# Kernel optimization log

Hardware: AMD Instinct MI355X
Metric: run time of the kernel (lower is better)

## Reference

```python
import jax, jax.numpy as jnp
import numpy as np
from math import factorial

NODES = 40000      # number of nodes
EDGES = 640000     # number of edges (avg degree 16)
MUL = 8            # multiplicity of each irrep in hidden (8x0e+8x1e+8x2e)
NB = 16            # radial basis size (radial_neurons[0])
MAXR = 3.0         # max_radius
NSPECIES = 8
DEG = 16.0         # num_neighbors normalization
R8 = 1.0 / np.sqrt(8.0)

# ---------- real Clebsch-Gordan coefficients (precomputed with numpy) ----------
def _clebsch(j1, m1, j2, m2, j3, m3):
    f = factorial
    if m1 + m2 != m3:
        return 0.0
    pref = ((2*j3+1) * f(j3+j1-j2) * f(j3-j1+j2) * f(j1+j2-j3) / f(j1+j2+j3+1)) ** 0.5
    pref *= (f(j3+m3)*f(j3-m3)*f(j1-m1)*f(j1+m1)*f(j2-m2)*f(j2+m2)) ** 0.5
    lo = max(0, j2-j3-m1, j1-j3+m2)
    hi = min(j1+j2-j3, j1-m1, j2+m2)
    s = 0.0
    for k in range(lo, hi+1):
        s += (-1)**k / (f(k)*f(j1+j2-j3-k)*f(j1-m1-k)*f(j2+m2-k)*f(j3-j2+m1+k)*f(j3-j1-m2+k))
    return pref * s

def _U(l):
    # complex -> real spherical-harmonic change of basis (rows: real m, cols: complex m)
    U = np.zeros((2*l+1, 2*l+1), dtype=complex)
    s2 = 2 ** -0.5
    for m in range(-l, l+1):
        if m > 0:
            U[m+l, m+l] = (-1)**m * s2; U[m+l, -m+l] = s2
        elif m == 0:
            U[l, l] = 1.0
        else:
            U[m+l, m+l] = 1j*s2; U[m+l, -m+l] = -1j*((-1)**m)*s2
    return U

def _real_cg(l1, l2, l3):
    C = np.zeros((2*l1+1, 2*l2+1, 2*l3+1))
    for m1 in range(-l1, l1+1):
        for m2 in range(-l2, l2+1):
            m3 = m1 + m2
            if abs(m3) <= l3:
                C[m1+l1, m2+l2, m3+l3] = _clebsch(l1, m1, l2, m2, l3, m3)
    T = np.einsum('am,bn,co,mno->abc', _U(l1).conj(), _U(l2).conj(), _U(l3), C)
    R = T.imag if np.abs(T.imag).max() > np.abs(T.real).max() else T.real
    return jnp.asarray(R.astype(np.float32))

PATHS = [(0,0,0),(0,1,1),(0,2,2),(1,0,1),(1,1,0),(1,1,1),(1,1,2),
         (1,2,1),(1,2,2),(2,0,2),(2,1,1),(2,1,2),(2,2,0),(2,2,1),(2,2,2)]
CG = {p: _real_cg(*p) for p in PATHS}
NIN = {0: 3.0, 1: 6.0, 2: 6.0}  # fan-in path counts per output l in hidden convs

# ---------- irrep feature layout: [.., 72] = 8x0e | 8x1e | 8x2e ----------
def _split(h):
    lead = h.shape[:-1]
    return (h[..., :MUL],
            h[..., MUL:4*MUL].reshape(lead + (MUL, 3)),
            h[..., 4*MUL:].reshape(lead + (MUL, 5)))

def _merge(s, v, t):
    lead = s.shape[:-1]
    return jnp.concatenate([s, v.reshape(lead + (3*MUL,)), t.reshape(lead + (5*MUL,))], -1)

def _act(h):
    # e3nn Activation: silu on 0e scalars, identity on l>0
    s, v, t = _split(h)
    return _merge(jax.nn.silu(s), v, t)

def _radial(emb, w1, b1, w2, b2):
    return jax.nn.silu(emb @ w1 + b1) @ w2 + b2

def _sh(u):
    # component-normalized real spherical harmonics l=0,1,2 of unit vectors u [E,3]
    x, y, z = u[:, 0], u[:, 1], u[:, 2]
    c15 = np.sqrt(15.0); c5 = np.sqrt(5.0); c3 = np.sqrt(3.0)
    y1 = jnp.stack([y, z, x], -1) * c3
    y2 = jnp.stack([c15*x*y, c15*y*z, 0.5*c5*(3*z*z - 1.0), c15*x*z, 0.5*c15*(x*x - y*y)], -1)
    return jnp.concatenate([jnp.ones_like(x)[:, None], y1, y2], -1)

def _soft_onehot(r):
    # e3nn soft_one_hot_linspace, basis='smooth_finite', cutoff=True
    values = jnp.linspace(0.0, MAXR, NB + 2)[1:-1]
    step = MAXR / (NB + 1)
    d = (r[:, None] - values) / step
    inside = jnp.abs(d) < 1.0
    dd = jnp.where(inside, d, 0.0)
    f = jnp.exp(-1.0 / (1.0 + dd)) * jnp.exp(-1.0 / (1.0 - dd))
    return 1.14136 * np.exp(2.0) * jnp.where(inside, f, 0.0)

def _tp_first(hs, sh, w):
    # uvu TP: 8x0e (x) SH(1x0e+1x1e+1x2e) -> hidden; hs [E,8], sh [E,9], w [E,3,8]
    m_s = w[:, 0] * hs * sh[:, :1]
    m_v = w[:, 1][..., None] * hs[..., None] * sh[:, None, 1:4]
    m_t = w[:, 2][..., None] * hs[..., None] * sh[:, None, 4:9]
    return _merge(m_s, m_v, m_t)

def _tp_uuu(h1, h2, w):
    # depthwise (uuu) CG tensor product hidden (x) hidden -> hidden; w [E,15,8]
    s1, v1, t1 = _split(h1); s2, v2, t2 = _split(h2)
    a = {0: s1[..., None], 1: v1, 2: t1}
    b = {0: s2[..., None], 1: v2, 2: t2}
    out = {0: 0.0, 1: 0.0, 2: 0.0}
    for p, (l1, l2, l3) in enumerate(PATHS):
        out[l3] = out[l3] + w[:, p, :, None] * jnp.einsum('eci,ecj,ijk->eck', a[l1], b[l2], CG[(l1, l2, l3)])
    return _merge(out[0][..., 0] / np.sqrt(NIN[0]), out[1] / np.sqrt(NIN[1]), out[2] / np.sqrt(NIN[2]))

def _lin_hidden(h, lin):
    # irrep-wise linear self-connection, lin [3,8,8]
    s, v, t = _split(h)
    return _merge(s @ lin[0] * R8,
                  jnp.einsum('ncm,cd->ndm', v, lin[1]) * R8,
                  jnp.einsum('ncm,cd->ndm', t, lin[2]) * R8)

def _model(x, edge_index, edge_vec, embed_w, lin0, lin1, lin2, out_w,
           r0_w1, r0_b1, r0_w2, r0_b2, r1_w1, r1_b1, r1_w2, r1_b2,
           r2_w1, r2_b1, r2_w2, r2_b2):
    src, dst = edge_index[0], edge_index[1]
    h = embed_w[x]                                   # [N, 8] scalar node feats
    r = jnp.sqrt(jnp.sum(edge_vec**2, -1) + 1e-12)
    emb = _soft_onehot(r)                            # [E, 16]
    hb_sh = _sh(edge_vec / r[:, None])               # [E, 9]
    rdeg = 1.0 / np.sqrt(DEG)
    # conv 0 + activation
    w = _radial(emb, r0_w1, r0_b1, r0_w2, r0_b2).reshape(-1, 3, MUL)
    m = _tp_first(h[src], hb_sh, w)                  # [E, 72]
    agg = jax.ops.segment_sum(m, dst, num_segments=NODES) * rdeg
    h = _act(agg.at[:, :MUL].add((h @ lin0) * R8))
    hb = _act(m)
    # convs 1..2 + activation
    for (w1, b1, w2, b2, lin) in ((r1_w1, r1_b1, r1_w2, r1_b2, lin1),
                                  (r2_w1, r2_b1, r2_w2, r2_b2, lin2)):
        w = _radial(emb, w1, b1, w2, b2).reshape(-1, 15, MUL)
        m = _tp_uuu(h[src], hb, w)
        agg = jax.ops.segment_sum(m, dst, num_segments=NODES) * rdeg
        h = _act(_lin_hidden(h, lin) + agg)
        hb = _act(m)
    # output FullyConnectedTensorProduct(h, h) -> 8x0e (paths l(x)l->0)
    s, v, t = _split(h)
    i0 = s[:, :, None] * s[:, None, :]
    i1 = jnp.einsum('nim,njm->nij', v, v) / np.sqrt(3.0)
    i2 = jnp.einsum('nim,njm->nij', t, t) / np.sqrt(5.0)
    out = (jnp.einsum('nij,ijk->nk', i0, out_w[0])
           + jnp.einsum('nij,ijk->nk', i1, out_w[1])
           + jnp.einsum('nij,ijk->nk', i2, out_w[2])) / np.sqrt(3.0 * MUL * MUL)
    return out

def setup_inputs() -> dict:
    key = jax.random.key(0)
    ks = jax.random.split(key, 16)
    inp = {}
    inp['x'] = jax.random.randint(ks[0], (NODES,), 0, NSPECIES)
    inp['edge_index'] = jax.random.randint(ks[1], (2, EDGES), 0, NODES)
    inp['edge_vec'] = jax.random.normal(ks[2], (EDGES, 3), dtype=jnp.float32)
    inp['embed_w'] = jax.random.normal(ks[3], (NSPECIES, MUL), dtype=jnp.float32)
    inp['lin0'] = jax.random.normal(ks[4], (MUL, MUL), dtype=jnp.float32)
    inp['lin1'] = jax.random.normal(ks[5], (3, MUL, MUL), dtype=jnp.float32)
    inp['lin2'] = jax.random.normal(ks[6], (3, MUL, MUL), dtype=jnp.float32)
    inp['out_w'] = jax.random.normal(ks[7], (3, MUL, MUL, MUL), dtype=jnp.float32)
    for i, (name, od) in enumerate((('r0', 3*MUL), ('r1', 15*MUL), ('r2', 15*MUL))):
        k1, k2 = jax.random.split(ks[8+i])
        inp[name+'_w1'] = jax.random.normal(k1, (NB, 64), dtype=jnp.float32) / np.sqrt(NB)
        inp[name+'_b1'] = jnp.zeros((64,), dtype=jnp.float32)
        inp[name+'_w2'] = jax.random.normal(k2, (64, od), dtype=jnp.float32) / 8.0
        inp[name+'_b2'] = jnp.zeros((od,), dtype=jnp.float32)
    return inp

def reference(x, edge_index, edge_vec, embed_w, lin0, lin1, lin2, out_w,
              r0_w1, r0_b1, r0_w2, r0_b2, r1_w1, r1_b1, r1_w2, r1_b2,
              r2_w1, r2_b1, r2_w2, r2_b2):
    return _model(x, edge_index, edge_vec, embed_w, lin0, lin1, lin2, out_w,
                  r0_w1, r0_b1, r0_w2, r0_b2, r1_w1, r1_b1, r1_w2, r1_b2,
                  r2_w1, r2_b1, r2_w2, r2_b2)
```

## Files before the change

### kernel.cpp

```cpp
#include <hip/hip_runtime.h>

#define NODES 40000
#define EDGES 640000

typedef float f32x2v __attribute__((ext_vector_type(2)));
typedef float f32x4v __attribute__((ext_vector_type(4)));
typedef short short8v __attribute__((ext_vector_type(8)));

__device__ __forceinline__ float silu_f(float x) { return x / (1.0f + __expf(-x)); }
__device__ __forceinline__ f32x2v mk2(float a, float b) { f32x2v r; r[0] = a; r[1] = b; return r; }

__device__ __forceinline__ void tp_uuu2(const f32x2v* wv,
                                        f32x2v as, const f32x2v* av, const f32x2v* at,
                                        f32x2v bs, const f32x2v* bv, const f32x2v* bt,
                                        f32x2v& ms, f32x2v* mv, f32x2v* mt)
{
    const float CR = 0.70710678f;
    const float K1 = 0.31622777f;
    const float K3 = 0.54772256f;
    const float KA = 0.40824829f;
    const float KB = 0.70710678f;
    const float KC = 0.81649658f;
    const float L4 = 0.63245553f;
    const float G2 = 0.53452248f;
    const float G1 = 0.26726124f;
    const float HH = 0.46291005f;

    f32x2v os = {0.f, 0.f};
    f32x2v ov0 = {0.f, 0.f}, ov1 = {0.f, 0.f}, ov2 = {0.f, 0.f};
    f32x2v ot0 = {0.f, 0.f}, ot1 = {0.f, 0.f}, ot2 = {0.f, 0.f};
    f32x2v ot3 = {0.f, 0.f}, ot4 = {0.f, 0.f};

    os += wv[0] * as * bs;
    ov0 += wv[1] * as * bv[0]; ov1 += wv[1] * as * bv[1]; ov2 += wv[1] * as * bv[2];
    ot0 += wv[2] * as * bt[0]; ot1 += wv[2] * as * bt[1]; ot2 += wv[2] * as * bt[2];
    ot3 += wv[2] * as * bt[3]; ot4 += wv[2] * as * bt[4];
    ov0 += wv[3] * av[0] * bs; ov1 += wv[3] * av[1] * bs; ov2 += wv[3] * av[2] * bs;
    os += wv[4] * (-0.57735027f) * (av[0]*bv[0] + av[1]*bv[1] + av[2]*bv[2]);
    ov0 += wv[5] * CR * (av[1]*bv[2] - av[2]*bv[1]);
    ov1 += wv[5] * CR * (av[2]*bv[0] - av[0]*bv[2]);
    ov2 += wv[5] * CR * (av[0]*bv[1] - av[1]*bv[0]);
    ot0 += wv[6] * CR * (av[2]*bv[0] + av[0]*bv[2]);
    ot1 += wv[6] * CR * (av[0]*bv[1] + av[1]*bv[0]);
    ot2 += wv[6] * 0.40824829f * (2.f*av[1]*bv[1] - av[2]*bv[2] - av[0]*bv[0]);
    ot3 += wv[6] * CR * (av[2]*bv[1] + av[1]*bv[2]);
    ot4 += wv[6] * CR * (av[2]*bv[2] - av[0]*bv[0]);
    ov0 += wv[7] * (-K3*av[1]*bt[1] + K1*av[0]*bt[2] - K3*av[2]*bt[0] + K3*av[0]*bt[4]);
    ov1 += wv[7] * (-2.f*K1*av[1]*bt[2] - K3*av[2]*bt[3] - K3*av[0]*bt[1]);
    ov2 += wv[7] * (-K3*av[1]*bt[3] + K1*av[2]*bt[2] - K3*av[0]*bt[0] - K3*av[2]*bt[4]);
    ot0 += wv[8] * ( KC*av[1]*bt[4] - KA*av[2]*bt[3] + KA*av[0]*bt[1]);
    ot1 += wv[8] * ( KA*av[1]*bt[3] - KB*av[2]*bt[2] - KA*av[0]*bt[0] - KA*av[2]*bt[4]);
    ot2 += wv[8] * ( KB*av[2]*bt[1] - KB*av[0]*bt[3]);
    ot3 += wv[8] * (-KA*av[1]*bt[1] + KB*av[0]*bt[2] + KA*av[2]*bt[0] - KA*av[0]*bt[4]);
    ot4 += wv[8] * (-KC*av[1]*bt[0] + KA*av[2]*bt[1] + KA*av[0]*bt[3]);
    ot0 += wv[9] * at[0] * bs; ot1 += wv[9] * at[1] * bs; ot2 += wv[9] * at[2] * bs;
    ot3 += wv[9] * at[3] * bs; ot4 += wv[9] * at[4] * bs;
    ov0 += wv[10] * (-K3*bv[1]*at[1] + K1*bv[0]*at[2] - K3*bv[2]*at[0] + K3*bv[0]*at[4]);
    ov1 += wv[10] * (-2.f*K1*bv[1]*at[2] - K3*bv[2]*at[3] - K3*bv[0]*at[1]);
    ov2 += wv[10] * (-K3*bv[1]*at[3] + K1*bv[2]*at[2] - K3*bv[0]*at[0] - K3*bv[2]*at[4]);
    ot0 -= wv[11] * ( KC*bv[1]*at[4] - KA*bv[2]*at[3] + KA*bv[0]*at[1]);
    ot1 -= wv[11] * ( KA*bv[1]*at[3] - KB*bv[2]*at[2] - KA*bv[0]*at[0] - KA*bv[2]*at[4]);
    ot2 -= wv[11] * ( KB*bv[2]*at[1] - KB*bv[0]*at[3]);
    ot3 -= wv[11] * (-KA*bv[1]*at[1] + KB*bv[0]*at[2] + KA*bv[2]*at[0] - KA*bv[0]*at[4]);
    ot4 -= wv[11] * (-KC*bv[1]*at[0] + KA*bv[2]*at[1] + KA*bv[0]*at[3]);
    os += wv[12] * 0.44721360f * (at[0]*bt[0] + at[1]*bt[1] + at[2]*bt[2] + at[3]*bt[3] + at[4]*bt[4]);
    ov0 += wv[13] * ( K1*(at[0]*bt[1] - at[1]*bt[0]) + K3*(at[3]*bt[2] - at[2]*bt[3]) + K1*(at[4]*bt[3] - at[3]*bt[4]) );
    ov1 += wv[13] * ( L4*(at[0]*bt[4] - at[4]*bt[0]) + K1*(at[1]*bt[3] - at[3]*bt[1]) );
    ov2 += wv[13] * ( K1*(at[3]*bt[0] - at[0]*bt[3]) + K3*(at[2]*bt[1] - at[1]*bt[2]) + K1*(at[4]*bt[1] - at[1]*bt[4]) );
    ot0 += wv[14] * ( G2*(at[2]*bt[0] + at[0]*bt[2]) - HH*(at[1]*bt[3] + at[3]*bt[1]) );
    ot1 += wv[14] * (-HH*(at[3]*bt[0] + at[0]*bt[3]) + HH*(at[1]*bt[4] + at[4]*bt[1]) - G1*(at[2]*bt[1] + at[1]*bt[2]) );
    ot2 += wv[14] * ( G2*(at[0]*bt[0] + at[4]*bt[4] - at[2]*bt[2]) - G1*(at[1]*bt[1] + at[3]*bt[3]) );
    ot3 += wv[14] * (-HH*(at[1]*bt[0] + at[0]*bt[1]) - HH*(at[3]*bt[4] + at[4]*bt[3]) - G1*(at[2]*bt[3] + at[3]*bt[2]) );
    ot4 += wv[14] * ( G2*(at[2]*bt[4] + at[4]*bt[2]) + HH*(at[1]*bt[1] - at[3]*bt[3]) );

    ms = os * 0.57735027f;
    mv[0] = ov0 * 0.40824829f; mv[1] = ov1 * 0.40824829f; mv[2] = ov2 * 0.40824829f;
    mt[0] = ot0 * 0.40824829f; mt[1] = ot1 * 0.40824829f; mt[2] = ot2 * 0.40824829f;
    mt[3] = ot3 * 0.40824829f; mt[4] = ot4 * 0.40824829f;
}

__global__ void deg_kernel(const int* __restrict__ eidx, int* __restrict__ deg)
{
    int e = blockIdx.x * 256 + threadIdx.x;
    if (e < EDGES) atomicAdd(&deg[eidx[EDGES + e]], 1);
}

__launch_bounds__(1024)
__global__ void scan_kernel(const int* __restrict__ deg, int* __restrict__ off,
                            int* __restrict__ cursor)
{
    __shared__ int part[1024];
    const int t = threadIdx.x;
    const int base = t * 40;
    int v[40];
    if (t < 1000) {
        const int4* p4 = (const int4*)(deg + base);
        #pragma unroll
        for (int i = 0; i < 10; ++i) {
            int4 q = p4[i];
            v[4 * i + 0] = q.x; v[4 * i + 1] = q.y;
            v[4 * i + 2] = q.z; v[4 * i + 3] = q.w;
        }
    } else {
        #pragma unroll
        for (int i = 0; i < 40; ++i) v[i] = 0;
    }
    int loc[40];
    int s = 0;
    #pragma unroll
    for (int i = 0; i < 40; ++i) { loc[i] = s; s += v[i]; }
    part[t] = s;
    __syncthreads();
    for (int d = 1; d < 1024; d <<= 1) {
        int vv = (t >= d) ? part[t - d] : 0;
        __syncthreads();
        part[t] += vv;
        __syncthreads();
    }
    int tb = (t == 0) ? 0 : part[t - 1];
    if (t < 1000) {
        #pragma unroll
        for (int i = 0; i < 40; ++i) {
            off[base + i] = tb + loc[i];
            cursor[base + i] = tb + loc[i];
        }
    }
    if (t == 1023) off[NODES] = part[1023];
}

__global__ void build_kernel(const int* __restrict__ eidx, const float* __restrict__ ev,
                             int* __restrict__ cursor,
                             float* __restrict__ evp, int* __restrict__ srcs)
{
    int e = blockIdx.x * 256 + threadIdx.x;
    if (e < EDGES) {
        int dst = eidx[EDGES + e];
        int p = atomicAdd(&cursor[dst], 1);
        srcs[p] = (int)(((unsigned)eidx[e]) | ((unsigned)dst << 16));
        evp[p * 3 + 0] = ev[e * 3 + 0];
        evp[p * 3 + 1] = ev[e * 3 + 1];
        evp[p * 3 + 2] = ev[e * 3 + 2];
    }
}

__launch_bounds__(256, 3)
__global__ void layer0_edge(const float* __restrict__ evp, const int* __restrict__ srcs,
                            const int* __restrict__ xs, const float* __restrict__ embw,
                            const float* __restrict__ w1, const float* __restrict__ b1,
                            const float* __restrict__ w2, const float* __restrict__ b2,
                            float* __restrict__ mbuf)
{
    __shared__ float emb_s[128 * 17];
    __shared__ float hid_s[128 * 68];
    __shared__ float w2t[24 * 68];
    const int tid = threadIdx.x;
    const int e0 = blockIdx.x * 128;

    for (int idx = tid; idx < 64 * 24; idx += 256) {
        int j = idx / 24, o = idx - j * 24;
        w2t[o * 68 + j] = w2[idx];
    }
    for (int idx = tid; idx < 2048; idx += 256) {
        int e = idx >> 4, i = idx & 15;
        const float* ep = evp + (size_t)(e0 + e) * 3;
        float ex = ep[0], ey = ep[1], ez = ep[2];
        float r = sqrtf(ex * ex + ey * ey + ez * ez + 1e-12f);
        float d = r * (17.0f / 3.0f) - (float)(i + 1);
        float f = 0.0f;
        if (fabsf(d) < 1.0f) f = 8.433572869f * __expf(-2.0f / (1.0f - d * d));
        emb_s[e * 17 + i] = f;
    }
    __syncthreads();

    {
        const int egp = tid >> 3;
        const int jb = (tid & 7) * 8;
        float acc2[4][8];
        #pragma unroll
        for (int el = 0; el < 4; ++el)
            #pragma unroll
            for (int k = 0; k < 8; ++k) acc2[el][k] = b1[jb + k];
        #pragma unroll
        for (int i = 0; i < 16; ++i) {
            float4 wa = *(const float4*)&w1[i * 64 + jb];
            float4 wb = *(const float4*)&w1[i * 64 + jb + 4];
            #pragma unroll
            for (int el = 0; el < 4; ++el) {
                float evv = emb_s[(egp * 4 + el) * 17 + i];
                acc2[el][0] += evv * wa.x; acc2[el][1] += evv * wa.y;
                acc2[el][2] += evv * wa.z; acc2[el][3] += evv * wa.w;
                acc2[el][4] += evv * wb.x; acc2[el][5] += evv * wb.y;
                acc2[el][6] += evv * wb.z; acc2[el][7] += evv * wb.w;
            }
        }
        #pragma unroll
        for (int el = 0; el < 4; ++el)
            #pragma unroll
            for (int k = 0; k < 8; ++k)
                hid_s[(egp * 4 + el) * 68 + jb + k] = silu_f(acc2[el][k]);
    }
    __syncthreads();

    const int c = tid & 7, g = (tid >> 3) & 7, wv_ = tid >> 6;
    float wacc[3][4];
    #pragma unroll
    for (int p = 0; p < 3; ++p) {
        float bb = b2[p * 8 + c];
        #pragma unroll
        for (int q = 0; q < 4; ++q) wacc[p][q] = bb;
    }
    for (int jb = 0; jb < 64; jb += 4) {
        float4 h4[4];
        #pragma unroll
        for (int q = 0; q < 4; ++q)
            h4[q] = *(const float4*)&hid_s[(wv_ * 32 + q * 8 + g) * 68 + jb];
        #pragma unroll
        for (int p = 0; p < 3; ++p) {
            float4 w4 = *(const float4*)&w2t[(p * 8 + c) * 68 + jb];
            #pragma unroll
            for (int q = 0; q < 4; ++q)
                wacc[p][q] += h4[q].x * w4.x + h4[q].y * w4.y + h4[q].z * w4.z + h4[q].w * w4.w;
        }
    }

    const int ebase = wv_ * 32 + g;
    #pragma unroll
    for (int q = 0; q < 4; ++q) {
        const int sl = e0 + ebase + 8 * q;
        const int sn = (int)((unsigned)srcs[sl] & 0xffffu);
        float hs = embw[xs[sn] * 8 + c];
        float* me = mbuf + (size_t)sl * 72;
        me[c]      = wacc[0][q] * hs;
        me[8 + c]  = wacc[1][q] * hs;
        me[16 + c] = wacc[2][q] * hs;
    }
}

__launch_bounds__(256, 3)
__global__ void tp_edge(const float* __restrict__ evp, const int* __restrict__ srcs,
                        const float* __restrict__ h,
                        const float* __restrict__ w1, const float* __restrict__ b1,
                        const float* __restrict__ w2, const float* __restrict__ b2,
                        float* __restrict__ mbuf, float* __restrict__ agg,
                        const int writeM, const int compactB)
{
    __shared__ float ws_t[120 * 68];
    __shared__ unsigned short hid_s[128 * 64];
    __shared__ int dst_s[66];
    float* emb_s = ws_t;

    const int tid = threadIdx.x;
    const int e0 = blockIdx.x * 128;

    for (int idx = tid; idx < 2048; idx += 256) {
        int e = idx >> 4, i = idx & 15;
        const float* ep = evp + (size_t)(e0 + e) * 3;
        float ex = ep[0], ey = ep[1], ez = ep[2];
        float r = sqrtf(ex * ex + ey * ey + ez * ez + 1e-12f);
        float d = r * (17.0f / 3.0f) - (float)(i + 1);
        float f = 0.0f;
        if (fabsf(d) < 1.0f) f = 8.433572869f * __expf(-2.0f / (1.0f - d * d));
        emb_s[e * 17 + i] = f;
    }
    __syncthreads();

    {
        const int egp = tid >> 3;
        const int jb = (tid & 7) * 8;
        f32x2v acc2[2][8];
        #pragma unroll
        for (int pr = 0; pr < 2; ++pr)
            #pragma unroll
            for (int k = 0; k < 8; ++k) { float bb = b1[jb + k]; acc2[pr][k] = mk2(bb, bb); }
        #pragma unroll
        for (int i = 0; i < 16; ++i) {
            float4 wa = *(const float4*)&w1[i * 64 + jb];
            float4 wb = *(const float4*)&w1[i * 64 + jb + 4];
            #pragma unroll
            for (int pr = 0; pr < 2; ++pr) {
                f32x2v evv = mk2(emb_s[(egp * 4 + 2 * pr) * 17 + i],
                                 emb_s[(egp * 4 + 2 * pr + 1) * 17 + i]);
                acc2[pr][0] += evv * wa.x; acc2[pr][1] += evv * wa.y;
                acc2[pr][2] += evv * wa.z; acc2[pr][3] += evv * wa.w;
                acc2[pr][4] += evv * wb.x; acc2[pr][5] += evv * wb.y;
                acc2[pr][6] += evv * wb.z; acc2[pr][7] += evv * wb.w;
            }
        }
        #pragma unroll
        for (int pr = 0; pr < 2; ++pr) {
            #pragma unroll
            for (int u = 0; u < 2; ++u) {
                unsigned int us[8];
                #pragma unroll
                for (int k = 0; k < 8; ++k) {
                    unsigned int b = __float_as_uint(silu_f(acc2[pr][k][u]));
                    b += 0x7fffu + ((b >> 16) & 1u);
                    us[k] = b >> 16;
                }
                uint4 pk;
                pk.x = us[0] | (us[1] << 16);
                pk.y = us[2] | (us[3] << 16);
                pk.z = us[4] | (us[5] << 16);
                pk.w = us[6] | (us[7] << 16);
                int rr = egp * 4 + 2 * pr + u;
                *(uint4*)&hid_s[rr * 64 + (jb ^ ((rr & 7) << 3))] = pk;
            }
        }
    }
    __syncthreads();

    const int l  = tid & 63;
    const int wq = tid >> 6;
    const int lr = l & 15;
    const int lg = l >> 4;

    short8v bhi[2][2], blo[2][2];
    #pragma unroll
    for (int n2 = 0; n2 < 2; ++n2) {
        int col  = (2 * wq + n2) * 16 + lr;
        int colc = col < 120 ? col : 119;
        #pragma unroll
        for (int ks = 0; ks < 2; ++ks) {
            short8v hv, lv;
            #pragma unroll
            for (int j = 0; j < 8; ++j) {
                int k = ks * 32 + lg * 8 + j;
                float v = w2[k * 120 + colc];
                if (col >= 120) v = 0.0f;
                unsigned bb = __float_as_uint(v);
                unsigned rh = bb + 0x7fffu + ((bb >> 16) & 1u);
                float hf = __uint_as_float((rh >> 16) << 16);
                unsigned bl = __float_as_uint(v - hf);
                bl += 0x7fffu + ((bl >> 16) & 1u);
                hv[j] = (short)(rh >> 16);
                lv[j] = (short)(bl >> 16);
            }
            bhi[n2][ks] = hv;
            blo[n2][ks] = lv;
        }
    }

    const int c = tid & 7, g = (tid >> 3) & 7, wv_ = tid >> 6;
    const int ebh = wv_ * 16 + g;

    #pragma unroll
    for (int half = 0; half < 2; ++half) {
        #pragma unroll
        for (int mm = 0; mm < 4; ++mm) {
            int e  = 64 * half + 16 * mm + lr;
            int sw = (e & 7) << 3;
            short8v a0 = *(const short8v*)&hid_s[e * 64 + ((lg * 8) ^ sw)];
            short8v a1 = *(const short8v*)&hid_s[e * 64 + ((32 + lg * 8) ^ sw)];
            #pragma unroll
            for (int n2 = 0; n2 < 2; ++n2) {
                int col = (2 * wq + n2) * 16 + lr;
                float bias = (col < 120) ? b2[col] : 0.0f;
                f32x4v acc;
                acc[0] = bias; acc[1] = bias; acc[2] = bias; acc[3] = bias;
                acc = __builtin_amdgcn_mfma_f32_16x16x32_bf16(a0, bhi[n2][0], acc, 0, 0, 0);
                acc = __builtin_amdgcn_mfma_f32_16x16x32_bf16(a1, bhi[n2][1], acc, 0, 0, 0);
                acc = __builtin_amdgcn_mfma_f32_16x16x32_bf16(a0, blo[n2][0], acc, 0, 0, 0);
                acc = __builtin_amdgcn_mfma_f32_16x16x32_bf16(a1, blo[n2][1], acc, 0, 0, 0);
                if (col < 120)
                    *(f32x4v*)&ws_t[col * 68 + 16 * mm + lg * 4] = acc;
            }
        }
        __syncthreads();

        {
            const int eA = e0 + 64 * half + ebh;
            const int eB = eA + 8;
            const unsigned pkA = (unsigned)srcs[eA], pkB = (unsigned)srcs[eB];
            const int snA = (int)(pkA & 0xffffu), snB = (int)(pkB & 0xffffu);
            const float* hn0 = h + (size_t)snA * 72 + c * 9;
            const float* hn1 = h + (size_t)snB * 72 + c * 9;

            f32x2v as = mk2(hn0[0], hn1[0]);
            f32x2v av[3], at[5], bv[3], bt[5], bs;
            #pragma unroll
            for (int i = 0; i < 3; ++i) av[i] = mk2(hn0[1 + i], hn1[1 + i]);
            #pragma unroll
            for (int i = 0; i < 5; ++i) at[i] = mk2(hn0[4 + i], hn1[4 + i]);

            if (compactB) {
                float w0A = mbuf[(size_t)eA * 72 + c];
                float w1A = mbuf[(size_t)eA * 72 + 8 + c];
                float w2A = mbuf[(size_t)eA * 72 + 16 + c];
                float w0B = mbuf[(size_t)eB * 72 + c];
                float w1B = mbuf[(size_t)eB * 72 + 8 + c];
                float w2B = mbuf[(size_t)eB * 72 + 16 + c];
                const float* epA = evp + (size_t)eA * 3;
                const float* epB = evp + (size_t)eB * 3;
                float exA = epA[0], eyA = epA[1], ezA = epA[2];
                float exB = epB[0], eyB = epB[1], ezB = epB[2];
                float rA = sqrtf(exA * exA + eyA * eyA + ezA * ezA + 1e-12f);
                float rB = sqrtf(exB * exB + eyB * eyB + ezB * ezB + 1e-12f);
                float iA = 1.0f / rA, iB = 1.0f / rB;
                float xA = exA * iA, yA = eyA * iA, zA = ezA * iA;
                float xB = exB * iB, yB = eyB * iB, zB = ezB * iB;
                const float c3 = 1.7320508f, c15 = 3.8729833f, c5 = 2.2360680f;
                bs = mk2(silu_f(w0A), silu_f(w0B));
                bv[0] = mk2(w1A * (c3 * yA), w1B * (c3 * yB));
                bv[1] = mk2(w1A * (c3 * zA), w1B * (c3 * zB));
                bv[2] = mk2(w1A * (c3 * xA), w1B * (c3 * xB));
                bt[0] = mk2(w2A * (c15 * xA * yA), w2B * (c15 * xB * yB));
                bt[1] = mk2(w2A * (c15 * yA * zA), w2B * (c15 * yB * zB));
                bt[2] = mk2(w2A * (0.5f * c5 * (3.f * zA * zA - 1.f)),
                            w2B * (0.5f * c5 * (3.f * zB * zB - 1.f)));
                bt[3] = mk2(w2A * (c15 * xA * zA), w2B * (c15 * xB * zB));
                bt[4] = mk2(w2A * (0.5f * c15 * (xA * xA - yA * yA)),
                            w2B * (0.5f * c15 * (xB * xB - yB * yB)));
            } else {
                const float* me0 = mbuf + (size_t)eA * 72 + c * 9;
                const float* me1 = mbuf + (size_t)eB * 72 + c * 9;
                bs = mk2(silu_f(me0[0]), silu_f(me1[0]));
                #pragma unroll
                for (int i = 0; i < 3; ++i) bv[i] = mk2(me0[1 + i], me1[1 + i]);
                #pragma unroll
                for (int i = 0; i < 5; ++i) bt[i] = mk2(me0[4 + i], me1[4 + i]);
            }

            f32x2v wvv[15];
            #pragma unroll
            for (int p = 0; p < 15; ++p)
                wvv[p] = mk2(ws_t[(p * 8 + c) * 68 + ebh],
                             ws_t[(p * 8 + c) * 68 + ebh + 8]);

            f32x2v ms, mv[3], mt[5];
            tp_uuu2(wvv, as, av, at, bs, bv, bt, ms, mv, mt);

            if (writeM) {
                float* mo0 = mbuf + (size_t)eA * 72 + c * 9;
                float* mo1 = mbuf + (size_t)eB * 72 + c * 9;
                mo0[0] = ms[0]; mo1[0] = ms[1];
                #pragma unroll
                for (int i = 0; i < 3; ++i) { mo0[1 + i] = mv[i][0]; mo1[1 + i] = mv[i][1]; }
                #pragma unroll
                for (int i = 0; i < 5; ++i) { mo0[4 + i] = mt[i][0]; mo1[4 + i] = mt[i][1]; }
            }

            if (tid <= 64) {
                int gs = e0 + 64 * half + tid;
                dst_s[tid] = (gs < EDGES) ? (int)((unsigned)srcs[gs] >> 16) : -1;
            }
            __syncthreads();

            float* m_s = ws_t;
            const int lA = ebh, lB = ebh + 8;
            m_s[lA * 72 + c * 9] = ms[0]; m_s[lB * 72 + c * 9] = ms[1];
            #pragma unroll
            for (int i = 0; i < 3; ++i) {
                m_s[lA * 72 + c * 9 + 1 + i] = mv[i][0];
                m_s[lB * 72 + c * 9 + 1 + i] = mv[i][1];
            }
            #pragma unroll
            for (int i = 0; i < 5; ++i) {
                m_s[lA * 72 + c * 9 + 4 + i] = mt[i][0];
                m_s[lB * 72 + c * 9 + 4 + i] = mt[i][1];
            }
            __syncthreads();

            if (tid < 216) {
                const int seg  = tid / 72;
                const int comp = tid - seg * 72;
                const int p0 = (seg == 0) ? 0  : ((seg == 1) ? 22 : 43);
                const int p1 = (seg == 0) ? 22 : ((seg == 1) ? 43 : 64);
                float sum = 0.f;
                int cur = dst_s[p0];
                for (int p = p0; p < p1; ++p) {
                    sum += m_s[p * 72 + comp];
                    int nxt = dst_s[p + 1];
                    if (nxt != cur) {
                        atomicAdd(&agg[(size_t)cur * 72 + comp], sum);
                        sum = 0.f; cur = nxt;
                    }
                }
                if (cur >= 0) atomicAdd(&agg[(size_t)cur * 72 + comp], sum);
            }
        }
        if (half == 0) __syncthreads();
    }
}

__global__ void node0(const int* __restrict__ xs, const float* __restrict__ embw,
                      const float* __restrict__ lin0, const float* __restrict__ mbuf,
                      const float* __restrict__ evp,
                      const int* __restrict__ off, float* __restrict__ h)
{
    int idx = blockIdx.x * 256 + threadIdx.x;
    int n = idx >> 3, c = idx & 7;
    int xb = xs[n] * 8;
    float dot = 0.f;
    #pragma unroll
    for (int d = 0; d < 8; ++d) dot += embw[xb + d] * lin0[d * 8 + c];

    float an[9];
    #pragma unroll
    for (int i = 0; i < 9; ++i) an[i] = 0.f;
    const float c3 = 1.7320508f, c15 = 3.8729833f, c5 = 2.2360680f;
    const int beg = off[n], end = off[n + 1];
    for (int p = beg; p < end; ++p) {
        float w0 = mbuf[(size_t)p * 72 + c];
        float w1 = mbuf[(size_t)p * 72 + 8 + c];
        float w2 = mbuf[(size_t)p * 72 + 16 + c];
        const float* ep = evp + (size_t)p * 3;
        float ex = ep[0], ey = ep[1], ez = ep[2];
        float r = sqrtf(ex * ex + ey * ey + ez * ez + 1e-12f);
        float inv = 1.0f / r;
        float x = ex * inv, y = ey * inv, z = ez * inv;
        an[0] += w0;
        an[1] += w1 * (c3 * y);
        an[2] += w1 * (c3 * z);
        an[3] += w1 * (c3 * x);
        an[4] += w2 * (c15 * x * y);
        an[5] += w2 * (c15 * y * z);
        an[6] += w2 * (0.5f * c5 * (3.f * z * z - 1.f));
        an[7] += w2 * (c15 * x * z);
        an[8] += w2 * (0.5f * c15 * (x * x - y * y));
    }

    float* hn = h + (size_t)n * 72 + c * 9;
    hn[0] = silu_f(an[0] * 0.25f + dot * 0.35355339f);
    #pragma unroll
    for (int i = 1; i < 9; ++i) hn[i] = an[i] * 0.25f;
}

__global__ void node12(const float* __restrict__ hin, const float* __restrict__ lin,
                       const float* __restrict__ agg, float* __restrict__ hout)
{
    int idx = blockIdx.x * 256 + threadIdx.x;
    int n = idx >> 3, d = idx & 7;

    float an[9];
    #pragma unroll
    for (int i = 0; i < 9; ++i) an[i] = agg[(size_t)n * 72 + d * 9 + i];

    const float* hn = hin + (size_t)n * 72;
    float* ho = hout + (size_t)n * 72 + d * 9;

    float s = 0.f;
    #pragma unroll
    for (int c = 0; c < 8; ++c) s += hn[c * 9] * lin[c * 8 + d];
    ho[0] = silu_f(s * 0.35355339f + an[0] * 0.25f);
    #pragma unroll
    for (int i = 0; i < 3; ++i) {
        float v = 0.f;
        #pragma unroll
        for (int c = 0; c < 8; ++c) v += hn[c * 9 + 1 + i] * lin[64 + c * 8 + d];
        ho[1 + i] = v * 0.35355339f + an[1 + i] * 0.25f;
    }
    #pragma unroll
    for (int i = 0; i < 5; ++i) {
        float t = 0.f;
        #pragma unroll
        for (int c = 0; c < 8; ++c) t += hn[c * 9 + 4 + i] * lin[128 + c * 8 + d];
        ho[4 + i] = t * 0.35355339f + an[4 + i] * 0.25f;
    }
}

__global__ void node12_out(const float* __restrict__ hin, const float* __restrict__ lin,
                           const float* __restrict__ agg,
                           const float* __restrict__ outw, float* __restrict__ out)
{
    __shared__ float hrec[32][72];
    int idx = blockIdx.x * 256 + threadIdx.x;
    int n = idx >> 3, d = idx & 7;
    int nl = threadIdx.x >> 3;

    float an[9];
    #pragma unroll
    for (int i = 0; i < 9; ++i) an[i] = agg[(size_t)n * 72 + d * 9 + i];

    const float* hn = hin + (size_t)n * 72;
    float* ho = &hrec[nl][d * 9];

    float s = 0.f;
    #pragma unroll
    for (int c = 0; c < 8; ++c) s += hn[c * 9] * lin[c * 8 + d];
    ho[0] = silu_f(s * 0.35355339f + an[0] * 0.25f);
    #pragma unroll
    for (int i = 0; i < 3; ++i) {
        float v = 0.f;
        #pragma unroll
        for (int c = 0; c < 8; ++c) v += hn[c * 9 + 1 + i] * lin[64 + c * 8 + d];
        ho[1 + i] = v * 0.35355339f + an[1 + i] * 0.25f;
    }
    #pragma unroll
    for (int i = 0; i < 5; ++i) {
        float t = 0.f;
        #pragma unroll
        for (int c = 0; c < 8; ++c) t += hn[c * 9 + 4 + i] * lin[128 + c * 8 + d];
        ho[4 + i] = t * 0.35355339f + an[4 + i] * 0.25f;
    }
    __syncthreads();

    const float* hr = &hrec[nl][0];
    float sv[8], vv[24], tv[40];
    #pragma unroll
    for (int i = 0; i < 8; ++i) {
        sv[i] = hr[i * 9];
        #pragma unroll
        for (int q = 0; q < 3; ++q) vv[i * 3 + q] = hr[i * 9 + 1 + q];
        #pragma unroll
        for (int q = 0; q < 5; ++q) tv[i * 5 + q] = hr[i * 9 + 4 + q];
    }
    float acc = 0.f;
    #pragma unroll
    for (int i = 0; i < 8; ++i) {
        #pragma unroll
        for (int j = 0; j < 8; ++j) {
            float dv = vv[i*3+0]*vv[j*3+0] + vv[i*3+1]*vv[j*3+1] + vv[i*3+2]*vv[j*3+2];
            float dt = tv[i*5+0]*tv[j*5+0] + tv[i*5+1]*tv[j*5+1] + tv[i*5+2]*tv[j*5+2]
                     + tv[i*5+3]*tv[j*5+3] + tv[i*5+4]*tv[j*5+4];
            int o = (i * 8 + j) * 8 + d;
            acc += sv[i] * sv[j] * outw[o]
                 + dv * 0.57735027f * outw[512 + o]
                 + dt * 0.44721360f * outw[1024 + o];
        }
    }
    out[n * 8 + d] = acc * 0.072168784f;
}

extern "C" void kernel_launch(void* const* d_in, const int* in_sizes, int n_in,
                              void* d_out, int out_size, void* d_ws, size_t ws_size,
                              hipStream_t stream)
{
    const int*   x    = (const int*)  d_in[0];
    const int*   eidx = (const int*)  d_in[1];
    const float* ev   = (const float*)d_in[2];
    const float* embw = (const float*)d_in[3];
    const float* lin0 = (const float*)d_in[4];
    const float* lin1 = (const float*)d_in[5];
    const float* lin2 = (const float*)d_in[6];
    const float* outw = (const float*)d_in[7];
    const float* r0w1 = (const float*)d_in[8];
    const float* r0b1 = (const float*)d_in[9];
    const float* r0w2 = (const float*)d_in[10];
    const float* r0b2 = (const float*)d_in[11];
    const float* r1w1 = (const float*)d_in[12];
    const float* r1b1 = (const float*)d_in[13];
    const float* r1w2 = (const float*)d_in[14];
    const float* r1b2 = (const float*)d_in[15];
    const float* r2w1 = (const float*)d_in[16];
    const float* r2b1 = (const float*)d_in[17];
    const float* r2w2 = (const float*)d_in[18];
    const float* r2b2 = (const float*)d_in[19];

    float* mbuf = (float*)d_ws;
    float* hA   = mbuf + (size_t)EDGES * 72;
    float* hB   = hA + (size_t)NODES * 72;
    float* evp  = hB + (size_t)NODES * 72;
    int*   deg    = (int*)(evp + (size_t)EDGES * 3);
    int*   off    = deg + NODES;
    int*   cursor = off + NODES + 1;
    int*   srcs   = cursor + NODES;

    const int EBI = (EDGES + 255) / 256;
    const int EB  = EDGES / 128;
    const int NBK = NODES * 8 / 256;
    const size_t HBYTES = (size_t)NODES * 72 * sizeof(float);

    hipMemsetAsync(deg, 0, NODES * sizeof(int), stream);
    hipMemsetAsync(hB, 0, HBYTES, stream);
    deg_kernel<<<EBI, 256, 0, stream>>>(eidx, deg);
    scan_kernel<<<1, 1024, 0, stream>>>(deg, off, cursor);
    build_kernel<<<EBI, 256, 0, stream>>>(eidx, ev, cursor, evp, srcs);

    layer0_edge<<<EB, 256, 0, stream>>>(evp, srcs, x, embw, r0w1, r0b1, r0w2, r0b2, mbuf);
    node0<<<NBK, 256, 0, stream>>>(x, embw, lin0, mbuf, evp, off, hA);

    tp_edge<<<EB, 256, 0, stream>>>(evp, srcs, hA, r1w1, r1b1, r1w2, r1b2, mbuf, hB, 1, 1);
    node12<<<NBK, 256, 0, stream>>>(hA, lin1, hB, hB);

    hipMemsetAsync(hA, 0, HBYTES, stream);
    tp_edge<<<EB, 256, 0, stream>>>(evp, srcs, hB, r2w1, r2b1, r2w2, r2b2, mbuf, hA, 0, 0);
    node12_out<<<NBK, 256, 0, stream>>>(hB, lin2, hA, outw, (float*)d_out);
}
```

Before: 666.4 us.

## Fuse layer-0 scatter aggregation into edge kernel and precompute bf16 weight splits

layer0_edge now builds the spherical-harmonic-weighted messages in shared memory and scatters them into per-node accumulators with a segmented atomic reduction. node0 then only reads the finished sums instead of gathering mbuf and recomputing the edge geometry per node. A small prep kernel converts the layer-1 and layer-2 radial w2 weights once into hi/lo bf16 split layouts, so each tp_edge block does vector loads instead of per-block strided loads and conversion. The cost is extra atomics plus two additional barriers per half-block in layer0, an extra memset and an extra launch.

```diff
diff --git a/kernel.cpp b/kernel.cpp
--- a/kernel.cpp
+++ b/kernel.cpp
@@ -143,16 +143,36 @@
     }
 }
 
+__global__ void prep_w2(const float* __restrict__ w2_1, const float* __restrict__ w2_2,
+                        unsigned short* __restrict__ w2bf)
+{
+    int idx = blockIdx.x * 256 + threadIdx.x;
+    if (idx >= 2 * 128 * 64) return;
+    int layer = idx >> 13;
+    int rem = idx & 8191;
+    int col = rem >> 6, k = rem & 63;
+    float v = 0.f;
+    if (col < 120) v = (layer ? w2_2 : w2_1)[k * 120 + col];
+    unsigned bb = __float_as_uint(v);
+    unsigned rh = bb + 0x7fffu + ((bb >> 16) & 1u);
+    float hf = __uint_as_float((rh >> 16) << 16);
+    unsigned bl = __float_as_uint(v - hf);
+    bl += 0x7fffu + ((bl >> 16) & 1u);
+    w2bf[layer * 16384 + col * 64 + k] = (unsigned short)(rh >> 16);
+    w2bf[layer * 16384 + 8192 + col * 64 + k] = (unsigned short)(bl >> 16);
+}
+
 __launch_bounds__(256, 3)
 __global__ void layer0_edge(const float* __restrict__ evp, const int* __restrict__ srcs,
                             const int* __restrict__ xs, const float* __restrict__ embw,
                             const float* __restrict__ w1, const float* __restrict__ b1,
                             const float* __restrict__ w2, const float* __restrict__ b2,
-                            float* __restrict__ mbuf)
+                            float* __restrict__ mbuf, float* __restrict__ agg)
 {
     __shared__ float emb_s[128 * 17];
     __shared__ float hid_s[128 * 68];
     __shared__ float w2t[24 * 68];
+    __shared__ int dst_s[66];
     const int tid = threadIdx.x;
     const int e0 = blockIdx.x * 128;
 
@@ -224,15 +244,70 @@
     }
 
     const int ebase = wv_ * 32 + g;
+    const float c3 = 1.7320508f, c15 = 3.8729833f, c5 = 2.2360680f;
+    float cw0[4], cw1[4], cw2[4];
     #pragma unroll
     for (int q = 0; q < 4; ++q) {
         const int sl = e0 + ebase + 8 * q;
         const int sn = (int)((unsigned)srcs[sl] & 0xffffu);
         float hs = embw[xs[sn] * 8 + c];
+        cw0[q] = wacc[0][q] * hs;
+        cw1[q] = wacc[1][q] * hs;
+        cw2[q] = wacc[2][q] * hs;
         float* me = mbuf + (size_t)sl * 72;
-        me[c]      = wacc[0][q] * hs;
-        me[8 + c]  = wacc[1][q] * hs;
-        me[16 + c] = wacc[2][q] * hs;
+        me[c] = cw0[q]; me[8 + c] = cw1[q]; me[16 + c] = cw2[q];
+    }
+    __syncthreads();
+
+    float* m_s = hid_s;
+    #pragma unroll
+    for (int half = 0; half < 2; ++half) {
+        if ((wv_ >> 1) == half) {
+            #pragma unroll
+            for (int q = 0; q < 4; ++q) {
+                const int el = (wv_ & 1) * 32 + g + 8 * q;
+                const int sl = e0 + 64 * half + el;
+                const float* ep = evp + (size_t)sl * 3;
+                float ex = ep[0], ey = ep[1], ez = ep[2];
+                float r = sqrtf(ex * ex + ey * ey + ez * ez + 1e-12f);
+                float inv = 1.0f / r;
+                float x = ex * inv, y = ey * inv, z = ez * inv;
+                float* ms_ = m_s + el * 72 + c * 9;
+                ms_[0] = cw0[q];
+                ms_[1] = cw1[q] * (c3 * y);
+                ms_[2] = cw1[q] * (c3 * z);
+                ms_[3] = cw1[q] * (c3 * x);
+                ms_[4] = cw2[q] * (c15 * x * y);
+                ms_[5] = cw2[q] * (c15 * y * z);
+                ms_[6] = cw2[q] * (0.5f * c5 * (3.f * z * z - 1.f));
+                ms_[7] = cw2[q] * (c15 * x * z);
+                ms_[8] = cw2[q] * (0.5f * c15 * (x * x - y * y));
+            }
+        }
+        if (tid <= 64) {
+            int gs = e0 + 64 * half + tid;
+            dst_s[tid] = (gs < EDGES) ? (int)((unsigned)srcs[gs] >> 16) : -1;
+        }
+        __syncthreads();
+
+        if (tid < 216) {
+            const int seg  = tid / 72;
+            const int comp = tid - seg * 72;
+            const int p0 = (seg == 0) ? 0  : ((seg == 1) ? 22 : 43);
+            const int p1 = (seg == 0) ? 22 : ((seg == 1) ? 43 : 64);
+            float sum = 0.f;
+            int cur = dst_s[p0];
+            for (int p = p0; p < p1; ++p) {
+                sum += m_s[p * 72 + comp];
+                int nxt = dst_s[p + 1];
+                if (nxt != cur) {
+                    atomicAdd(&agg[(size_t)cur * 72 + comp], sum);
+                    sum = 0.f; cur = nxt;
+                }
+            }
+            if (cur >= 0) atomicAdd(&agg[(size_t)cur * 72 + comp], sum);
+        }
+        __syncthreads();
     }
 }
 
@@ -240,7 +315,7 @@
 __global__ void tp_edge(const float* __restrict__ evp, const int* __restrict__ srcs,
                         const float* __restrict__ h,
                         const float* __restrict__ w1, const float* __restrict__ b1,
-                        const float* __restrict__ w2, const float* __restrict__ b2,
+                        const unsigned short* __restrict__ w2bf, const float* __restrict__ b2,
                         float* __restrict__ mbuf, float* __restrict__ agg,
                         const int writeM, const int compactB)
 {
@@ -317,26 +392,11 @@
     short8v bhi[2][2], blo[2][2];
     #pragma unroll
     for (int n2 = 0; n2 < 2; ++n2) {
-        int col  = (2 * wq + n2) * 16 + lr;
-        int colc = col < 120 ? col : 119;
+        int col = (2 * wq + n2) * 16 + lr;
         #pragma unroll
         for (int ks = 0; ks < 2; ++ks) {
-            short8v hv, lv;
-            #pragma unroll
-            for (int j = 0; j < 8; ++j) {
-                int k = ks * 32 + lg * 8 + j;
-                float v = w2[k * 120 + colc];
-                if (col >= 120) v = 0.0f;
-                unsigned bb = __float_as_uint(v);
-                unsigned rh = bb + 0x7fffu + ((bb >> 16) & 1u);
-                float hf = __uint_as_float((rh >> 16) << 16);
-                unsigned bl = __float_as_uint(v - hf);
-                bl += 0x7fffu + ((bl >> 16) & 1u);
-                hv[j] = (short)(rh >> 16);
-                lv[j] = (short)(bl >> 16);
-            }
-            bhi[n2][ks] = hv;
-            blo[n2][ks] = lv;
+            bhi[n2][ks] = *(const short8v*)&w2bf[col * 64 + ks * 32 + lg * 8];
+            blo[n2][ks] = *(const short8v*)&w2bf[8192 + col * 64 + ks * 32 + lg * 8];
         }
     }
 
@@ -483,9 +543,8 @@
 }
 
 __global__ void node0(const int* __restrict__ xs, const float* __restrict__ embw,
-                      const float* __restrict__ lin0, const float* __restrict__ mbuf,
-                      const float* __restrict__ evp,
-                      const int* __restrict__ off, float* __restrict__ h)
+                      const float* __restrict__ lin0, const float* __restrict__ agg,
+                      float* __restrict__ h)
 {
     int idx = blockIdx.x * 256 + threadIdx.x;
     int n = idx >> 3, c = idx & 7;
@@ -496,28 +555,7 @@
 
     float an[9];
     #pragma unroll
-    for (int i = 0; i < 9; ++i) an[i] = 0.f;
-    const float c3 = 1.7320508f, c15 = 3.8729833f, c5 = 2.2360680f;
-    const int beg = off[n], end = off[n + 1];
-    for (int p = beg; p < end; ++p) {
-        float w0 = mbuf[(size_t)p * 72 + c];
-        float w1 = mbuf[(size_t)p * 72 + 8 + c];
-        float w2 = mbuf[(size_t)p * 72 + 16 + c];
-        const float* ep = evp + (size_t)p * 3;
-        float ex = ep[0], ey = ep[1], ez = ep[2];
-        float r = sqrtf(ex * ex + ey * ey + ez * ez + 1e-12f);
-        float inv = 1.0f / r;
-        float x = ex * inv, y = ey * inv, z = ez * inv;
-        an[0] += w0;
-        an[1] += w1 * (c3 * y);
-        an[2] += w1 * (c3 * z);
-        an[3] += w1 * (c3 * x);
-        an[4] += w2 * (c15 * x * y);
-        an[5] += w2 * (c15 * y * z);
-        an[6] += w2 * (0.5f * c5 * (3.f * z * z - 1.f));
-        an[7] += w2 * (c15 * x * z);
-        an[8] += w2 * (0.5f * c15 * (x * x - y * y));
-    }
+    for (int i = 0; i < 9; ++i) an[i] = agg[(size_t)n * 72 + c * 9 + i];
 
     float* hn = h + (size_t)n * 72 + c * 9;
     hn[0] = silu_f(an[0] * 0.25f + dot * 0.35355339f);
@@ -654,6 +692,7 @@
     int*   off    = deg + NODES;
     int*   cursor = off + NODES + 1;
     int*   srcs   = cursor + NODES;
+    unsigned short* w2bf = (unsigned short*)((((size_t)(srcs + EDGES)) + 15) & ~(size_t)15);
 
     const int EBI = (EDGES + 255) / 256;
     const int EB  = EDGES / 128;
@@ -661,18 +700,20 @@
     const size_t HBYTES = (size_t)NODES * 72 * sizeof(float);
 
     hipMemsetAsync(deg, 0, NODES * sizeof(int), stream);
+    hipMemsetAsync(hA, 0, HBYTES, stream);
     hipMemsetAsync(hB, 0, HBYTES, stream);
     deg_kernel<<<EBI, 256, 0, stream>>>(eidx, deg);
     scan_kernel<<<1, 1024, 0, stream>>>(deg, off, cursor);
     build_kernel<<<EBI, 256, 0, stream>>>(eidx, ev, cursor, evp, srcs);
-
-    layer0_edge<<<EB, 256, 0, stream>>>(evp, srcs, x, embw, r0w1, r0b1, r0w2, r0b2, mbuf);
-    node0<<<NBK, 256, 0, stream>>>(x, embw, lin0, mbuf, evp, off, hA);
-
-    tp_edge<<<EB, 256, 0, stream>>>(evp, srcs, hA, r1w1, r1b1, r1w2, r1b2, mbuf, hB, 1, 1);
+    prep_w2<<<64, 256, 0, stream>>>(r1w2, r2w2, w2bf);
+
+    layer0_edge<<<EB, 256, 0, stream>>>(evp, srcs, x, embw, r0w1, r0b1, r0w2, r0b2, mbuf, hA);
+    node0<<<NBK, 256, 0, stream>>>(x, embw, lin0, hA, hA);
+
+    tp_edge<<<EB, 256, 0, stream>>>(evp, srcs, hA, r1w1, r1b1, w2bf, r1b2, mbuf, hB, 1, 1);
     node12<<<NBK, 256, 0, stream>>>(hA, lin1, hB, hB);
 
     hipMemsetAsync(hA, 0, HBYTES, stream);
-    tp_edge<<<EB, 256, 0, stream>>>(evp, srcs, hB, r2w1, r2b1, r2w2, r2b2, mbuf, hA, 0, 0);
+    tp_edge<<<EB, 256, 0, stream>>>(evp, srcs, hB, r2w1, r2b1, w2bf + 16384, r2b2, mbuf, hA, 0, 0);
     node12_out<<<NBK, 256, 0, stream>>>(hB, lin2, hA, outw, (float*)d_out);
 }
```

Result: slower. 707.0 us (+6.1%).
